# Performance work log

Measured on AMD Instinct MI355X. Metric: run time of the kernel, lower is better.

The kernel has to match this reference:

```python
import jax, jax.numpy as jnp
import numpy as np

T, H, I, E = 8192, 1024, 2816, 8


def setup_inputs() -> dict:
    key = jax.random.key(0)
    k1, k2, k3, k4, k5 = jax.random.split(key, 5)
    s_in = 1.0 / np.sqrt(H)
    s_mid = 1.0 / np.sqrt(I)
    return {
        "x": jax.random.normal(k1, (T, H), dtype=jnp.float32),
        "expert_indices": jax.random.randint(k2, (T,), 0, E),
        "Wg": jax.random.normal(k3, (E, I, H), dtype=jnp.float32) * s_in,
        "Wu": jax.random.normal(k4, (E, I, H), dtype=jnp.float32) * s_in,
        "Wd": jax.random.normal(k5, (E, H, I), dtype=jnp.float32) * s_mid,
    }


def reference(x, expert_indices, Wg, Wu, Wd):
    # Faithful to TPMoEExperts.forward: per-expert 0/1 mask, dense SwiGLU MLP
    # over the full (masked) token batch, masked accumulate into output.
    output = jnp.zeros_like(x)
    for e in range(E):  # small fixed loop over experts (structurally distinct weights)
        mask = (expert_indices == e).astype(x.dtype)[:, None]  # [T,1]
        xi = x * mask                                           # [T,H]
        gate = jax.nn.silu(xi @ Wg[e].T)                        # [T,I]
        up = xi @ Wu[e].T                                       # [T,I]
        out_e = (gate * up) @ Wd[e].T                           # [T,H]
        output = output + out_e * mask
    return output
```

## Files before the change

### kernel.cpp

```cpp
#include <hip/hip_runtime.h>
#include <hip/hip_bf16.h>

#define T_TOK 8192
#define H_DIM 1024
#define I_DIM 2816
#define E_EXP 8

#define BK 32
#define MAXT (T_TOK / 256 + E_EXP)
#define GU_COLS (I_DIM / 128)
#define DN_COLS (H_DIM / 128)

typedef __bf16 bf16x8 __attribute__((ext_vector_type(8)));
typedef float f32x4 __attribute__((ext_vector_type(4)));

#define SWZ32(r, bc) (((r) * 64) + ((bc) ^ ((((r) >> 1) & 3) << 4)))

__device__ __forceinline__ void gload16(const void* g, void* l) {
  __builtin_amdgcn_global_load_lds((const __attribute__((address_space(1))) void*)g,
                                   (__attribute__((address_space(3))) void*)l, 16, 0, 0);
}

__device__ __forceinline__ bf16x8 cvt8(const float4& p0, const float4& p1) {
  bf16x8 v;
  v[0] = (__bf16)p0.x; v[1] = (__bf16)p0.y; v[2] = (__bf16)p0.z; v[3] = (__bf16)p0.w;
  v[4] = (__bf16)p1.x; v[5] = (__bf16)p1.y; v[6] = (__bf16)p1.z; v[7] = (__bf16)p1.w;
  return v;
}

__device__ __forceinline__ int xcd_swizzle(int id, int nwg) {
  const int q = nwg >> 3, r = nwg & 7;
  const int xcd = id & 7, j = id >> 3;
  return (xcd < r ? xcd * (q + 1) : r * (q + 1) + (xcd - r) * q) + j;
}

__global__ void k_count(const int* __restrict__ idx, int* __restrict__ counts) {
  int t = blockIdx.x * blockDim.x + threadIdx.x;
  if (t < T_TOK) atomicAdd(&counts[idx[t]], 1);
}

__global__ void k_tilesB(const int* __restrict__ counts, int* __restrict__ offsets,
                         int* __restrict__ tE, int* __restrict__ tB,
                         int* __restrict__ tEnd, int* __restrict__ nT) {
  if (threadIdx.x != 0 || blockIdx.x != 0) return;
  int off = 0, nt = 0;
  for (int e = 0; e < E_EXP; ++e) {
    offsets[e] = off;
    int c = counts[e];
    for (int b = 0; b < c; b += 256) { tE[nt] = e; tB[nt] = off + b; tEnd[nt] = off + c; ++nt; }
    off += c;
  }
  offsets[E_EXP] = off;
  *nT = nt;
}

__global__ void k_scatter(const int* __restrict__ idx, const int* __restrict__ offsets,
                          int* __restrict__ cursor, int* __restrict__ order) {
  int t = blockIdx.x * blockDim.x + threadIdx.x;
  if (t < T_TOK) {
    int e = idx[t];
    int p = offsets[e] + atomicAdd(&cursor[e], 1);
    order[p] = t;
  }
}

__global__ __launch_bounds__(256) void k_cvt3(const float* __restrict__ s0, const float* __restrict__ s1,
                                              const float* __restrict__ s2, __bf16* __restrict__ d0,
                                              __bf16* __restrict__ d1, __bf16* __restrict__ d2, int n8each) {
  int i = blockIdx.x * blockDim.x + threadIdx.x;
  int seg = i / n8each;
  int j = i - seg * n8each;
  if (seg >= 3) return;
  const float* s = seg == 0 ? s0 : (seg == 1 ? s1 : s2);
  __bf16* d = seg == 0 ? d0 : (seg == 1 ? d1 : d2);
  const float4 p0 = ((const float4*)s)[j * 2];
  const float4 p1 = ((const float4*)s)[j * 2 + 1];
  ((bf16x8*)d)[j] = cvt8(p0, p1);
}

__global__ __launch_bounds__(128) void k_xperm(const float* __restrict__ x,
                                               const int* __restrict__ order,
                                               __bf16* __restrict__ xp) {
  const int row = blockIdx.x;
  const int tok = order[row];
  const float* s = x + (size_t)tok * H_DIM + threadIdx.x * 8;
  const float4 p0 = ((const float4*)s)[0];
  const float4 p1 = ((const float4*)s)[1];
  *(bf16x8*)(xp + (size_t)row * H_DIM + threadIdx.x * 8) = cvt8(p0, p1);
}

__global__ __launch_bounds__(512) void k_gateup8(
    const __bf16* __restrict__ xp, const __bf16* __restrict__ wg, const __bf16* __restrict__ wu,
    const int* __restrict__ tE, const int* __restrict__ tB,
    const int* __restrict__ tEnd, const int* __restrict__ nT, __bf16* __restrict__ hp) {
  const int nwg = *nT * GU_COLS;
  const int id = blockIdx.x;
  if (id >= nwg) return;
  const int wgid = xcd_swizzle(id, nwg);
  const int tile = wgid / GU_COLS;
  const int col = wgid - tile * GU_COLS;
  const int e = tE[tile];
  const int rowbase = tB[tile];
  const int rowEnd = tEnd[tile];
  const int nbase = col * 128;

  extern __shared__ __align__(16) unsigned char smem[];
  unsigned char* smA = smem;
  unsigned char* smG = smem + 32768;
  unsigned char* smU = smem + 49152;

  const int tid = threadIdx.x;
  const int lane = tid & 63;
  const int w = tid >> 6;
  const int wm = w & 3, wn = w >> 2;

  const int srow = tid >> 2;
  const int sch = (tid & 3) ^ ((tid >> 3) & 3);
  const __bf16* aS0 = xp + (size_t)(rowbase + srow) * H_DIM + sch * 8;
  const __bf16* aS1 = xp + (size_t)(rowbase + 128 + srow) * H_DIM + sch * 8;
  const __bf16* gS = wg + ((size_t)e * I_DIM + nbase + srow) * H_DIM + sch * 8;
  const __bf16* uS = wu + ((size_t)e * I_DIM + nbase + srow) * H_DIM + sch * 8;
  const int ldst = tid * 16;

  f32x4 accg[4][4], accu[4][4];
#pragma unroll
  for (int m = 0; m < 4; ++m)
#pragma unroll
    for (int n = 0; n < 4; ++n)
#pragma unroll
      for (int j = 0; j < 4; ++j) { accg[m][n][j] = 0.f; accu[m][n][j] = 0.f; }

  auto STAGE = [&](int kt, int b) {
    const size_t kof = (size_t)kt * BK;
    gload16(aS0 + kof, smA + b * 16384 + ldst);
    gload16(aS1 + kof, smA + b * 16384 + 8192 + ldst);
    gload16(gS + kof, smG + b * 8192 + ldst);
    gload16(uS + kof, smU + b * 8192 + ldst);
  };

  const int nK = H_DIM / BK;
  STAGE(0, 0);
  __syncthreads();

  int cur = 0;
  const int kc = (lane >> 4) * 16;
  for (int kt = 0; kt < nK; ++kt) {
    if (kt + 1 < nK) STAGE(kt + 1, cur ^ 1);
    const unsigned char* A = smA + cur * 16384;
    const unsigned char* G = smG + cur * 8192;
    const unsigned char* U = smU + cur * 8192;
    bf16x8 a[4], bg[4], bu[4];
#pragma unroll
    for (int m = 0; m < 4; ++m)
      a[m] = *(const bf16x8*)(A + SWZ32(wm * 64 + m * 16 + (lane & 15), kc));
#pragma unroll
    for (int n = 0; n < 4; ++n) {
      const int off = SWZ32(wn * 64 + n * 16 + (lane & 15), kc);
      bg[n] = *(const bf16x8*)(G + off);
      bu[n] = *(const bf16x8*)(U + off);
    }
#pragma unroll
    for (int m = 0; m < 4; ++m)
#pragma unroll
      for (int n = 0; n < 4; ++n) {
        accg[m][n] = __builtin_amdgcn_mfma_f32_16x16x32_bf16(a[m], bg[n], accg[m][n], 0, 0, 0);
        accu[m][n] = __builtin_amdgcn_mfma_f32_16x16x32_bf16(a[m], bu[n], accu[m][n], 0, 0, 0);
      }
    __syncthreads();
    cur ^= 1;
  }

#pragma unroll
  for (int m = 0; m < 4; ++m) {
    const int row0 = wm * 64 + m * 16 + (lane >> 4) * 4;
#pragma unroll
    for (int j = 0; j < 4; ++j) {
      const int gr = rowbase + row0 + j;
      if (gr < rowEnd) {
        __bf16* dst = hp + (size_t)gr * I_DIM + nbase;
#pragma unroll
        for (int n = 0; n < 4; ++n) {
          const int c2 = wn * 64 + n * 16 + (lane & 15);
          const float g = accg[m][n][j];
          const float u = accu[m][n][j];
          dst[c2] = (__bf16)(g / (1.f + __expf(-g)) * u);
        }
      }
    }
  }
}

__global__ __launch_bounds__(512) void k_down8(
    const __bf16* __restrict__ hp, const __bf16* __restrict__ wd,
    const int* __restrict__ order, const int* __restrict__ tE, const int* __restrict__ tB,
    const int* __restrict__ tEnd, const int* __restrict__ nT, float* __restrict__ out) {
  const int nwg = *nT * DN_COLS;
  const int id = blockIdx.x;
  if (id >= nwg) return;
  const int wgid = xcd_swizzle(id, nwg);
  const int tile = wgid >> 3;
  const int col = wgid & 7;
  const int e = tE[tile];
  const int rowbase = tB[tile];
  const int rowEnd = tEnd[tile];
  const int nbase = col * 128;

  __shared__ __align__(16) unsigned char smA[2][16384];
  __shared__ __align__(16) unsigned char smB[2][8192];

  const int tid = threadIdx.x;
  const int lane = tid & 63;
  const int w = tid >> 6;
  const int wm = w & 3, wn = w >> 2;

  const int srow = tid >> 2;
  const int sch = (tid & 3) ^ ((tid >> 3) & 3);
  const __bf16* aS0 = hp + (size_t)(rowbase + srow) * I_DIM + sch * 8;
  const __bf16* aS1 = hp + (size_t)(rowbase + 128 + srow) * I_DIM + sch * 8;
  const __bf16* bS = wd + ((size_t)e * H_DIM + nbase + srow) * I_DIM + sch * 8;
  const int ldst = tid * 16;

  f32x4 acc[4][4];
#pragma unroll
  for (int m = 0; m < 4; ++m)
#pragma unroll
    for (int n = 0; n < 4; ++n)
#pragma unroll
      for (int j = 0; j < 4; ++j) acc[m][n][j] = 0.f;

  auto STAGE = [&](int kt, int b) {
    const size_t kof = (size_t)kt * BK;
    gload16(aS0 + kof, &smA[b][0] + ldst);
    gload16(aS1 + kof, &smA[b][0] + 8192 + ldst);
    gload16(bS + kof, &smB[b][0] + ldst);
  };

  const int nK = I_DIM / BK;
  STAGE(0, 0);
  __syncthreads();

  int cur = 0;
  const int kc = (lane >> 4) * 16;
  for (int kt = 0; kt < nK; ++kt) {
    if (kt + 1 < nK) STAGE(kt + 1, cur ^ 1);
    const unsigned char* A = &smA[cur][0];
    const unsigned char* B = &smB[cur][0];
    bf16x8 a[4], b[4];
#pragma unroll
    for (int m = 0; m < 4; ++m)
      a[m] = *(const bf16x8*)(A + SWZ32(wm * 64 + m * 16 + (lane & 15), kc));
#pragma unroll
    for (int n = 0; n < 4; ++n)
      b[n] = *(const bf16x8*)(B + SWZ32(wn * 64 + n * 16 + (lane & 15), kc));
#pragma unroll
    for (int m = 0; m < 4; ++m)
#pragma unroll
      for (int n = 0; n < 4; ++n)
        acc[m][n] = __builtin_amdgcn_mfma_f32_16x16x32_bf16(a[m], b[n], acc[m][n], 0, 0, 0);
    __syncthreads();
    cur ^= 1;
  }

#pragma unroll
  for (int m = 0; m < 4; ++m) {
    const int row0 = wm * 64 + m * 16 + (lane >> 4) * 4;
#pragma unroll
    for (int j = 0; j < 4; ++j) {
      const int gr = rowbase + row0 + j;
      if (gr < rowEnd) {
        const int tok = order[gr];
        float* dst = out + (size_t)tok * H_DIM + nbase;
#pragma unroll
        for (int n = 0; n < 4; ++n) {
          const int c2 = wn * 64 + n * 16 + (lane & 15);
          dst[c2] = acc[m][n][j];
        }
      }
    }
  }
}

extern "C" void kernel_launch(void* const* d_in, const int* in_sizes, int n_in,
                              void* d_out, int out_size, void* d_ws, size_t ws_size,
                              hipStream_t stream) {
  const float* x = (const float*)d_in[0];
  const int* eidx = (const int*)d_in[1];
  const float* Wg = (const float*)d_in[2];
  const float* Wu = (const float*)d_in[3];
  const float* Wd = (const float*)d_in[4];
  float* out = (float*)d_out;

  char* ws = (char*)d_ws;
  size_t off = 0;
  auto alloc = [&](size_t bytes) -> void* {
    void* p = ws + off;
    off = (off + bytes + 255) & ~(size_t)255;
    return p;
  };
  const size_t TPAD = T_TOK + 256;
  __bf16* hp = (__bf16*)alloc(TPAD * I_DIM * sizeof(__bf16));
  int* order = (int*)alloc(T_TOK * sizeof(int));
  int* offsets = (int*)alloc((E_EXP + 1) * sizeof(int));
  int* tE = (int*)alloc(MAXT * sizeof(int));
  int* tB = (int*)alloc(MAXT * sizeof(int));
  int* tEnd = (int*)alloc(MAXT * sizeof(int));
  int* nT = (int*)alloc(sizeof(int));
  int* cc = (int*)alloc(2 * E_EXP * sizeof(int));
  int* counts = cc;
  int* cursor = cc + E_EXP;

  const size_t WSZ = (size_t)E_EXP * I_DIM * H_DIM;
  __bf16* xp = (__bf16*)alloc(TPAD * H_DIM * sizeof(__bf16));
  __bf16* wg16 = (__bf16*)alloc(WSZ * sizeof(__bf16));
  __bf16* wu16 = (__bf16*)alloc(WSZ * sizeof(__bf16));
  __bf16* wd16 = (__bf16*)alloc(WSZ * sizeof(__bf16));

  hipFuncSetAttribute((const void*)k_gateup8,
                      hipFuncAttributeMaxDynamicSharedMemorySize, 65536);

  hipMemsetAsync(cc, 0, 2 * E_EXP * sizeof(int), stream);
  k_count<<<T_TOK / 256, 256, 0, stream>>>(eidx, counts);
  k_tilesB<<<1, 1, 0, stream>>>(counts, offsets, tE, tB, tEnd, nT);
  k_scatter<<<T_TOK / 256, 256, 0, stream>>>(eidx, offsets, cursor, order);

  const int n8 = (int)(WSZ / 8);
  k_cvt3<<<(3 * n8 + 255) / 256, 256, 0, stream>>>(Wg, Wu, Wd, wg16, wu16, wd16, n8);
  k_xperm<<<T_TOK, 128, 0, stream>>>(x, order, xp);

  k_gateup8<<<GU_COLS * MAXT, 512, 65536, stream>>>(xp, wg16, wu16, tE, tB, tEnd, nT, hp);
  k_down8<<<DN_COLS * MAXT, 512, 0, stream>>>(hp, wd16, order, tE, tB, tEnd, nT, out);
}
```

Measured before the change: 381.8 us.

## Interleave gate/up weights and deepen GEMM K-pipeline with split-half staging

Gate and up weights are converted into one interleaved bf16 tensor in 16-row groups, so the gate-up GEMM runs as a single 256x256 tile with paired gate/up accumulators, which raises MFMA work per shared-memory load. Both GEMMs move to BK=64 split into two 32-wide halves. The loop uses explicit vmcnt waits and raw barriers in place of __syncthreads, plus s_setprio around the MFMA block, so loads overlap compute more finely. The change enlarges LDS use (128KB and 96KB), which lowers occupancy, and changes the down kernel's wave layout to 4x2.

```diff
diff --git a/kernel.cpp b/kernel.cpp
--- a/kernel.cpp
+++ b/kernel.cpp
@@ -6,15 +6,12 @@
 #define I_DIM 2816
 #define E_EXP 8
 
-#define BK 32
 #define MAXT (T_TOK / 256 + E_EXP)
-#define GU_COLS (I_DIM / 128)
-#define DN_COLS (H_DIM / 128)
+#define GU_COLS 22
+#define DN_COLS 8
 
 typedef __bf16 bf16x8 __attribute__((ext_vector_type(8)));
 typedef float f32x4 __attribute__((ext_vector_type(4)));
-
-#define SWZ32(r, bc) (((r) * 64) + ((bc) ^ ((((r) >> 1) & 3) << 4)))
 
 __device__ __forceinline__ void gload16(const void* g, void* l) {
   __builtin_amdgcn_global_load_lds((const __attribute__((address_space(1))) void*)g,
@@ -32,6 +29,13 @@
   const int q = nwg >> 3, r = nwg & 7;
   const int xcd = id & 7, j = id >> 3;
   return (xcd < r ? xcd * (q + 1) : r * (q + 1) + (xcd - r) * q) + j;
+}
+
+#define FENCE() asm volatile("" ::: "memory")
+#define BARRIER() do { __builtin_amdgcn_s_barrier(); FENCE(); } while (0)
+
+__device__ __forceinline__ int swz_off(int row, int lane) {
+  return row * 64 + ((((lane >> 4)) ^ ((row >> 1) & 3)) << 4);
 }
 
 __global__ void k_count(const int* __restrict__ idx, int* __restrict__ counts) {
@@ -64,18 +68,30 @@
   }
 }
 
-__global__ __launch_bounds__(256) void k_cvt3(const float* __restrict__ s0, const float* __restrict__ s1,
-                                              const float* __restrict__ s2, __bf16* __restrict__ d0,
-                                              __bf16* __restrict__ d1, __bf16* __restrict__ d2, int n8each) {
+__global__ __launch_bounds__(256) void k_cvt(const float* __restrict__ src,
+                                             __bf16* __restrict__ dst, int n8) {
   int i = blockIdx.x * blockDim.x + threadIdx.x;
-  int seg = i / n8each;
-  int j = i - seg * n8each;
-  if (seg >= 3) return;
-  const float* s = seg == 0 ? s0 : (seg == 1 ? s1 : s2);
-  __bf16* d = seg == 0 ? d0 : (seg == 1 ? d1 : d2);
-  const float4 p0 = ((const float4*)s)[j * 2];
-  const float4 p1 = ((const float4*)s)[j * 2 + 1];
-  ((bf16x8*)d)[j] = cvt8(p0, p1);
+  if (i < n8) {
+    const float4 p0 = ((const float4*)src)[i * 2];
+    const float4 p1 = ((const float4*)src)[i * 2 + 1];
+    ((bf16x8*)dst)[i] = cvt8(p0, p1);
+  }
+}
+
+__global__ __launch_bounds__(128) void k_cvtgu(const float* __restrict__ Wg,
+                                               const float* __restrict__ Wu,
+                                               __bf16* __restrict__ wgu) {
+  const int b = blockIdx.x;
+  const int e = b / I_DIM, i = b - e * I_DIM;
+  const int vg = ((i >> 4) << 5) + (i & 15);
+  const size_t sb = ((size_t)e * I_DIM + i) * H_DIM + threadIdx.x * 8;
+  const size_t db = ((size_t)e * (2 * I_DIM) + vg) * H_DIM + threadIdx.x * 8;
+  const float4 g0 = *(const float4*)(Wg + sb);
+  const float4 g1 = *(const float4*)(Wg + sb + 4);
+  *(bf16x8*)(wgu + db) = cvt8(g0, g1);
+  const float4 u0 = *(const float4*)(Wu + sb);
+  const float4 u1 = *(const float4*)(Wu + sb + 4);
+  *(bf16x8*)(wgu + db + (size_t)16 * H_DIM) = cvt8(u0, u1);
 }
 
 __global__ __launch_bounds__(128) void k_xperm(const float* __restrict__ x,
@@ -89,8 +105,8 @@
   *(bf16x8*)(xp + (size_t)row * H_DIM + threadIdx.x * 8) = cvt8(p0, p1);
 }
 
-__global__ __launch_bounds__(512) void k_gateup8(
-    const __bf16* __restrict__ xp, const __bf16* __restrict__ wg, const __bf16* __restrict__ wu,
+__global__ __launch_bounds__(512) void k_gateup10(
+    const __bf16* __restrict__ xp, const __bf16* __restrict__ wgu,
     const int* __restrict__ tE, const int* __restrict__ tB,
     const int* __restrict__ tEnd, const int* __restrict__ nT, __bf16* __restrict__ hp) {
   const int nwg = *nT * GU_COLS;
@@ -102,95 +118,102 @@
   const int e = tE[tile];
   const int rowbase = tB[tile];
   const int rowEnd = tEnd[tile];
-  const int nbase = col * 128;
 
   extern __shared__ __align__(16) unsigned char smem[];
   unsigned char* smA = smem;
-  unsigned char* smG = smem + 32768;
-  unsigned char* smU = smem + 49152;
+  unsigned char* smW = smem + 65536;
 
   const int tid = threadIdx.x;
   const int lane = tid & 63;
   const int w = tid >> 6;
-  const int wm = w & 3, wn = w >> 2;
+  const int wm = w >> 2, wn = w & 3;
 
   const int srow = tid >> 2;
   const int sch = (tid & 3) ^ ((tid >> 3) & 3);
   const __bf16* aS0 = xp + (size_t)(rowbase + srow) * H_DIM + sch * 8;
-  const __bf16* aS1 = xp + (size_t)(rowbase + 128 + srow) * H_DIM + sch * 8;
-  const __bf16* gS = wg + ((size_t)e * I_DIM + nbase + srow) * H_DIM + sch * 8;
-  const __bf16* uS = wu + ((size_t)e * I_DIM + nbase + srow) * H_DIM + sch * 8;
+  const __bf16* aS1 = aS0 + (size_t)128 * H_DIM;
+  const __bf16* wS0 = wgu + ((size_t)e * (2 * I_DIM) + col * 256 + srow) * H_DIM + sch * 8;
+  const __bf16* wS1 = wS0 + (size_t)128 * H_DIM;
   const int ldst = tid * 16;
 
-  f32x4 accg[4][4], accu[4][4];
-#pragma unroll
-  for (int m = 0; m < 4; ++m)
+  f32x4 acc[8][4];
+#pragma unroll
+  for (int m = 0; m < 8; ++m)
 #pragma unroll
     for (int n = 0; n < 4; ++n)
 #pragma unroll
-      for (int j = 0; j < 4; ++j) { accg[m][n][j] = 0.f; accu[m][n][j] = 0.f; }
-
-  auto STAGE = [&](int kt, int b) {
-    const size_t kof = (size_t)kt * BK;
-    gload16(aS0 + kof, smA + b * 16384 + ldst);
-    gload16(aS1 + kof, smA + b * 16384 + 8192 + ldst);
-    gload16(gS + kof, smG + b * 8192 + ldst);
-    gload16(uS + kof, smU + b * 8192 + ldst);
-  };
-
-  const int nK = H_DIM / BK;
+      for (int j = 0; j < 4; ++j) acc[m][n][j] = 0.f;
+
+  auto STAGE = [&](int t1, int kh) {
+    const int b = t1 & 1;
+    const size_t ko = (size_t)t1 * 64 + kh * 32;
+    const int lb = (b * 2 + kh) * 16384;
+    gload16(aS0 + ko, smA + lb + ldst);
+    gload16(aS1 + ko, smA + lb + 8192 + ldst);
+    gload16(wS0 + ko, smW + lb + ldst);
+    gload16(wS1 + ko, smW + lb + 8192 + ldst);
+  };
+
+  auto COMPUTE = [&](int buf, int kh) {
+    const unsigned char* A = smA + (buf * 2 + kh) * 16384;
+    const unsigned char* W = smW + (buf * 2 + kh) * 16384;
+    bf16x8 a[8], b[4];
+#pragma unroll
+    for (int m = 0; m < 8; ++m)
+      a[m] = *(const bf16x8*)(A + swz_off(wm * 128 + m * 16 + (lane & 15), lane));
+#pragma unroll
+    for (int n = 0; n < 4; ++n)
+      b[n] = *(const bf16x8*)(W + swz_off(wn * 64 + n * 16 + (lane & 15), lane));
+    __builtin_amdgcn_s_setprio(1);
+#pragma unroll
+    for (int m = 0; m < 8; ++m)
+#pragma unroll
+      for (int n = 0; n < 4; ++n)
+        acc[m][n] = __builtin_amdgcn_mfma_f32_16x16x32_bf16(a[m], b[n], acc[m][n], 0, 0, 0);
+    __builtin_amdgcn_s_setprio(0);
+  };
+
+  const int nK = H_DIM / 64;
   STAGE(0, 0);
-  __syncthreads();
-
-  int cur = 0;
-  const int kc = (lane >> 4) * 16;
-  for (int kt = 0; kt < nK; ++kt) {
-    if (kt + 1 < nK) STAGE(kt + 1, cur ^ 1);
-    const unsigned char* A = smA + cur * 16384;
-    const unsigned char* G = smG + cur * 8192;
-    const unsigned char* U = smU + cur * 8192;
-    bf16x8 a[4], bg[4], bu[4];
-#pragma unroll
-    for (int m = 0; m < 4; ++m)
-      a[m] = *(const bf16x8*)(A + SWZ32(wm * 64 + m * 16 + (lane & 15), kc));
-#pragma unroll
-    for (int n = 0; n < 4; ++n) {
-      const int off = SWZ32(wn * 64 + n * 16 + (lane & 15), kc);
-      bg[n] = *(const bf16x8*)(G + off);
-      bu[n] = *(const bf16x8*)(U + off);
-    }
-#pragma unroll
-    for (int m = 0; m < 4; ++m)
-#pragma unroll
-      for (int n = 0; n < 4; ++n) {
-        accg[m][n] = __builtin_amdgcn_mfma_f32_16x16x32_bf16(a[m], bg[n], accg[m][n], 0, 0, 0);
-        accu[m][n] = __builtin_amdgcn_mfma_f32_16x16x32_bf16(a[m], bu[n], accu[m][n], 0, 0, 0);
-      }
-    __syncthreads();
-    cur ^= 1;
-  }
-
-#pragma unroll
-  for (int m = 0; m < 4; ++m) {
-    const int row0 = wm * 64 + m * 16 + (lane >> 4) * 4;
+  STAGE(0, 1);
+  asm volatile("s_waitcnt vmcnt(4)" ::: "memory");
+  BARRIER();
+
+  for (int t = 0; t < nK; ++t) {
+    const int buf = t & 1;
+    const bool pf = (t + 1 < nK);
+    if (pf) STAGE(t + 1, 0);
+    COMPUTE(buf, 0);
+    if (pf) asm volatile("s_waitcnt vmcnt(4)" ::: "memory");
+    else    asm volatile("s_waitcnt vmcnt(0)" ::: "memory");
+    BARRIER();
+    if (pf) STAGE(t + 1, 1);
+    COMPUTE(buf, 1);
+    if (pf) asm volatile("s_waitcnt vmcnt(4)" ::: "memory");
+    else    asm volatile("s_waitcnt vmcnt(0)" ::: "memory");
+    BARRIER();
+  }
+
+#pragma unroll
+  for (int m = 0; m < 8; ++m) {
+    const int row0 = wm * 128 + m * 16 + ((lane >> 4) << 2);
 #pragma unroll
     for (int j = 0; j < 4; ++j) {
       const int gr = rowbase + row0 + j;
       if (gr < rowEnd) {
-        __bf16* dst = hp + (size_t)gr * I_DIM + nbase;
-#pragma unroll
-        for (int n = 0; n < 4; ++n) {
-          const int c2 = wn * 64 + n * 16 + (lane & 15);
-          const float g = accg[m][n][j];
-          const float u = accu[m][n][j];
-          dst[c2] = (__bf16)(g / (1.f + __expf(-g)) * u);
+        __bf16* dst = hp + (size_t)gr * I_DIM + col * 128 + wn * 32 + (lane & 15);
+#pragma unroll
+        for (int p = 0; p < 2; ++p) {
+          const float g = acc[m][2 * p][j];
+          const float u = acc[m][2 * p + 1][j];
+          dst[p * 16] = (__bf16)(g / (1.f + __expf(-g)) * u);
         }
       }
     }
   }
 }
 
-__global__ __launch_bounds__(512) void k_down8(
+__global__ __launch_bounds__(512) void k_down10(
     const __bf16* __restrict__ hp, const __bf16* __restrict__ wd,
     const int* __restrict__ order, const int* __restrict__ tE, const int* __restrict__ tB,
     const int* __restrict__ tEnd, const int* __restrict__ nT, float* __restrict__ out) {
@@ -205,19 +228,20 @@
   const int rowEnd = tEnd[tile];
   const int nbase = col * 128;
 
-  __shared__ __align__(16) unsigned char smA[2][16384];
-  __shared__ __align__(16) unsigned char smB[2][8192];
+  extern __shared__ __align__(16) unsigned char smem2[];
+  unsigned char* smA = smem2;
+  unsigned char* smW = smem2 + 65536;
 
   const int tid = threadIdx.x;
   const int lane = tid & 63;
   const int w = tid >> 6;
-  const int wm = w & 3, wn = w >> 2;
+  const int wm = w >> 1, wn = w & 1;
 
   const int srow = tid >> 2;
   const int sch = (tid & 3) ^ ((tid >> 3) & 3);
   const __bf16* aS0 = hp + (size_t)(rowbase + srow) * I_DIM + sch * 8;
-  const __bf16* aS1 = hp + (size_t)(rowbase + 128 + srow) * I_DIM + sch * 8;
-  const __bf16* bS = wd + ((size_t)e * H_DIM + nbase + srow) * I_DIM + sch * 8;
+  const __bf16* aS1 = aS0 + (size_t)128 * I_DIM;
+  const __bf16* wS = wd + ((size_t)e * H_DIM + nbase + srow) * I_DIM + sch * 8;
   const int ldst = tid * 16;
 
   f32x4 acc[4][4];
@@ -228,42 +252,57 @@
 #pragma unroll
       for (int j = 0; j < 4; ++j) acc[m][n][j] = 0.f;
 
-  auto STAGE = [&](int kt, int b) {
-    const size_t kof = (size_t)kt * BK;
-    gload16(aS0 + kof, &smA[b][0] + ldst);
-    gload16(aS1 + kof, &smA[b][0] + 8192 + ldst);
-    gload16(bS + kof, &smB[b][0] + ldst);
-  };
-
-  const int nK = I_DIM / BK;
-  STAGE(0, 0);
-  __syncthreads();
-
-  int cur = 0;
-  const int kc = (lane >> 4) * 16;
-  for (int kt = 0; kt < nK; ++kt) {
-    if (kt + 1 < nK) STAGE(kt + 1, cur ^ 1);
-    const unsigned char* A = &smA[cur][0];
-    const unsigned char* B = &smB[cur][0];
+  auto STAGE = [&](int t1, int kh) {
+    const int b = t1 & 1;
+    const size_t ko = (size_t)t1 * 64 + kh * 32;
+    gload16(aS0 + ko, smA + (b * 2 + kh) * 16384 + ldst);
+    gload16(aS1 + ko, smA + (b * 2 + kh) * 16384 + 8192 + ldst);
+    gload16(wS + ko, smW + (b * 2 + kh) * 8192 + ldst);
+  };
+
+  auto COMPUTE = [&](int buf, int kh) {
+    const unsigned char* A = smA + (buf * 2 + kh) * 16384;
+    const unsigned char* W = smW + (buf * 2 + kh) * 8192;
     bf16x8 a[4], b[4];
 #pragma unroll
     for (int m = 0; m < 4; ++m)
-      a[m] = *(const bf16x8*)(A + SWZ32(wm * 64 + m * 16 + (lane & 15), kc));
+      a[m] = *(const bf16x8*)(A + swz_off(wm * 64 + m * 16 + (lane & 15), lane));
 #pragma unroll
     for (int n = 0; n < 4; ++n)
-      b[n] = *(const bf16x8*)(B + SWZ32(wn * 64 + n * 16 + (lane & 15), kc));
+      b[n] = *(const bf16x8*)(W + swz_off(wn * 64 + n * 16 + (lane & 15), lane));
+    __builtin_amdgcn_s_setprio(1);
 #pragma unroll
     for (int m = 0; m < 4; ++m)
 #pragma unroll
       for (int n = 0; n < 4; ++n)
         acc[m][n] = __builtin_amdgcn_mfma_f32_16x16x32_bf16(a[m], b[n], acc[m][n], 0, 0, 0);
-    __syncthreads();
-    cur ^= 1;
+    __builtin_amdgcn_s_setprio(0);
+  };
+
+  const int nK = I_DIM / 64;
+  STAGE(0, 0);
+  STAGE(0, 1);
+  asm volatile("s_waitcnt vmcnt(3)" ::: "memory");
+  BARRIER();
+
+  for (int t = 0; t < nK; ++t) {
+    const int buf = t & 1;
+    const bool pf = (t + 1 < nK);
+    if (pf) STAGE(t + 1, 0);
+    COMPUTE(buf, 0);
+    if (pf) asm volatile("s_waitcnt vmcnt(3)" ::: "memory");
+    else    asm volatile("s_waitcnt vmcnt(0)" ::: "memory");
+    BARRIER();
+    if (pf) STAGE(t + 1, 1);
+    COMPUTE(buf, 1);
+    if (pf) asm volatile("s_waitcnt vmcnt(3)" ::: "memory");
+    else    asm volatile("s_waitcnt vmcnt(0)" ::: "memory");
+    BARRIER();
   }
 
 #pragma unroll
   for (int m = 0; m < 4; ++m) {
-    const int row0 = wm * 64 + m * 16 + (lane >> 4) * 4;
+    const int row0 = wm * 64 + m * 16 + ((lane >> 4) << 2);
 #pragma unroll
     for (int j = 0; j < 4; ++j) {
       const int gr = rowbase + row0 + j;
@@ -311,22 +350,24 @@
 
   const size_t WSZ = (size_t)E_EXP * I_DIM * H_DIM;
   __bf16* xp = (__bf16*)alloc(TPAD * H_DIM * sizeof(__bf16));
-  __bf16* wg16 = (__bf16*)alloc(WSZ * sizeof(__bf16));
-  __bf16* wu16 = (__bf16*)alloc(WSZ * sizeof(__bf16));
+  __bf16* wgu16 = (__bf16*)alloc(2 * WSZ * sizeof(__bf16));
   __bf16* wd16 = (__bf16*)alloc(WSZ * sizeof(__bf16));
 
-  hipFuncSetAttribute((const void*)k_gateup8,
-                      hipFuncAttributeMaxDynamicSharedMemorySize, 65536);
+  hipFuncSetAttribute((const void*)k_gateup10,
+                      hipFuncAttributeMaxDynamicSharedMemorySize, 131072);
+  hipFuncSetAttribute((const void*)k_down10,
+                      hipFuncAttributeMaxDynamicSharedMemorySize, 98304);
 
   hipMemsetAsync(cc, 0, 2 * E_EXP * sizeof(int), stream);
   k_count<<<T_TOK / 256, 256, 0, stream>>>(eidx, counts);
   k_tilesB<<<1, 1, 0, stream>>>(counts, offsets, tE, tB, tEnd, nT);
   k_scatter<<<T_TOK / 256, 256, 0, stream>>>(eidx, offsets, cursor, order);
 
+  k_cvtgu<<<E_EXP * I_DIM, 128, 0, stream>>>(Wg, Wu, wgu16);
   const int n8 = (int)(WSZ / 8);
-  k_cvt3<<<(3 * n8 + 255) / 256, 256, 0, stream>>>(Wg, Wu, Wd, wg16, wu16, wd16, n8);
+  k_cvt<<<(n8 + 255) / 256, 256, 0, stream>>>(Wd, wd16, n8);
   k_xperm<<<T_TOK, 128, 0, stream>>>(x, order, xp);
 
-  k_gateup8<<<GU_COLS * MAXT, 512, 65536, stream>>>(xp, wg16, wu16, tE, tB, tEnd, nT, hp);
-  k_down8<<<DN_COLS * MAXT, 512, 0, stream>>>(hp, wd16, order, tE, tB, tEnd, nT, out);
-}
+  k_gateup10<<<MAXT * GU_COLS, 512, 131072, stream>>>(xp, wgu16, tE, tB, tEnd, nT, hp);
+  k_down10<<<MAXT * DN_COLS, 512, 98304, stream>>>(hp, wd16, order, tE, tB, tEnd, nT, out);
+}
```

After: 375.3 us. About the same (-1.7%).
